# Kernel optimization log

Hardware: AMD Instinct MI355X
Metric: run time of the kernel (lower is better)

The kernel has to match this reference:

```python
import jax, jax.numpy as jnp
import numpy as np

B, L, CIN, COUT, TEMB, N_MODES = 32, 8192, 64, 64, 256, 64
M = N_MODES // 2 + 1  # retained rfft modes = 33
EPS = 1e-5


def setup_inputs() -> dict:
    key = jax.random.key(0)
    ks = jax.random.split(key, 12)
    std_w = float(np.sqrt(1.0 / (2.0 * CIN)))
    # flax Dense default kernel init = lecun_normal ~ normal(std=1/sqrt(fan_in)); plain normal is fine for a reference
    return {
        "x": jax.random.normal(ks[0], (B, L, CIN), jnp.float32),
        "t_emb": jax.random.normal(ks[1], (B, TEMB), jnp.float32),
        # SpectralFreqTimeConv1D params
        "spec_w_real": jax.random.normal(ks[2], (M, CIN, COUT), jnp.float32) * std_w,
        "spec_w_imag": jax.random.normal(ks[3], (M, CIN, COUT), jnp.float32) * std_w,
        "dense_re": jax.random.normal(ks[4], (TEMB, M), jnp.float32) / np.sqrt(TEMB),
        "dense_im": jax.random.normal(ks[5], (TEMB, M), jnp.float32) / np.sqrt(TEMB),
        # TimeConv1D params
        "conv_kernel": jax.random.normal(ks[6], (CIN, COUT), jnp.float32) / np.sqrt(CIN),
        "conv_bias": jnp.zeros((COUT,), jnp.float32),
        "tc_weights": jax.random.normal(ks[7], (COUT, COUT), jnp.float32) * 0.01,  # nn.initializers.normal() stddev=0.01
        "psi_kernel": jax.random.normal(ks[8], (TEMB, 2 * COUT), jnp.float32) / np.sqrt(TEMB),
        # BatchNorm params
        "bn_scale": jnp.ones((COUT,), jnp.float32),
        "bn_bias": jnp.zeros((COUT,), jnp.float32),
    }


def reference(x, t_emb, spec_w_real, spec_w_imag, dense_re, dense_im,
              conv_kernel, conv_bias, tc_weights, psi_kernel, bn_scale, bn_bias):
    b, L_in, _ = x.shape
    n_freq = L_in // 2 + 1

    # ---- SpectralFreqTimeConv1D ----
    x_ft = jnp.fft.rfft(x, axis=-2, norm="forward")            # (b, n_freq, CIN) complex
    t_c = (t_emb @ dense_re) + 1j * (t_emb @ dense_im)         # (b, M) complex
    W = spec_w_real + 1j * spec_w_imag                          # (M, CIN, COUT) complex
    # diagonal-in-mode modulation: equivalent to the eye-based einsum chain
    out_m = t_c[:, :, None] * jnp.einsum("bmi,mio->bmo", x_ft[:, :M, :], W)  # (b, M, COUT)
    out_ft = jnp.zeros((b, n_freq, COUT), jnp.complex64).at[:, :M, :].set(out_m)
    x_spec = jnp.fft.irfft(out_ft, axis=-2, n=L_in, norm="forward")  # (b, L, COUT)

    # ---- TimeConv1D (residual branch) ----
    h = x @ conv_kernel + conv_bias                             # 1x1 conv: (b, L, COUT)
    psi = t_emb @ psi_kernel                                    # (b, 2*COUT)
    w_t, b_t = jnp.split(psi, 2, axis=-1)
    # einsum('ij,bjk,blk->bli', W, diag(w_t), h) == (h * w_t) @ W^T
    x_res = jnp.einsum("blj,ij->bli", h * w_t[:, None, :], tc_weights) + b_t[:, None, :]

    # ---- combine, batchnorm (training: batch stats), activation ----
    out = x_spec + x_res
    mean = out.mean(axis=(0, 1))
    var = out.var(axis=(0, 1))
    out = (out - mean) * jax.lax.rsqrt(var + EPS) * bn_scale + bn_bias
    return jax.nn.relu(out)
```

## Files before the change

### kernel.cpp

```cpp
#include <hip/hip_runtime.h>
#include <hip/hip_fp16.h>

typedef short short8 __attribute__((ext_vector_type(8)));
typedef float f32x4 __attribute__((ext_vector_type(4)));
typedef unsigned int u32;
typedef u32 u32x4 __attribute__((ext_vector_type(4)));
typedef unsigned short u16;

#define BB 32
#define LL 8192
#define TE 256
#define MM 33
#define INVL (1.0f/8192.0f)

#define TBLM_OFF 0
#define TTD_OFF  262144
#define VTB_OFF  589824
#define DD_OFF   720896
#define DD2_OFF  722944
#define BNP_OFF  731200

#define SRED2_OFF 4227072
#define VF_OFF    4491264

static __device__ __forceinline__ u16 f2b(float f) {
  u32 u = __float_as_uint(f);
  return (u16)((u + 0x7FFFu + ((u >> 16) & 1u)) >> 16);
}
static __device__ __forceinline__ u32 pk2(float lo, float hi) {
  return __builtin_amdgcn_perm(__float_as_uint(hi) + 0x8000u,
                               __float_as_uint(lo) + 0x8000u,
                               0x07060302u);
}
static __device__ __forceinline__ float fsin(float rev) {
  float r; asm("v_sin_f32 %0, %1" : "=v"(r) : "v"(rev)); return r;
}
static __device__ __forceinline__ float fcos(float rev) {
  float r; asm("v_cos_f32 %0, %1" : "=v"(r) : "v"(rev)); return r;
}


__global__ __launch_bounds__(256) void k_tbl(float* __restrict__ ws) {
  u16* tt = (u16*)ws + TTD_OFF * 2;
  int t = blockIdx.x * 256 + threadIdx.x;
  int m = (t >> 13) + 1, l = t & (LL - 1);
  float rev = (float)((m * l) & (LL - 1)) * INVL;
  int js = (m == 32) ? 0 : 32 + m;
  tt[m * LL + l]  = f2b(fcos(rev));
  tt[js * LL + l] = f2b(fsin(rev));
}

__global__ __launch_bounds__(512) void k_dft(const float* __restrict__ x,
                                             const float* __restrict__ ws,
                                             float* __restrict__ scr) {
  __shared__ __align__(16) u16 sX[2][64 * 136];
  __shared__ float sOnes[8 * 64];
  int tid = threadIdx.x;
  int b = blockIdx.x >> 5, chunk = blockIdx.x & 31;
  int l0 = chunk * 256;
  int w = tid >> 6, lane = tid & 63;
  const u16* tt = (const u16*)ws + TTD_OFF * 2;

  f32x4 acc[4];
#pragma unroll
  for (int ct = 0; ct < 4; ++ct) acc[ct] = (f32x4){0.f, 0.f, 0.f, 0.f};

  int arow = lane & 15;
  int kb = (lane >> 4) * 8;
  bool isg = (w >= 4);
  int gi = w - 4;
  int sc = tid & 63, lg = tid >> 6;

  float vx[16];
  float psum = 0.f;
#pragma unroll
  for (int i = 0; i < 16; ++i)
    vx[i] = x[(b * LL + l0 + lg * 16 + i) * 64 + sc];
  {
    u32 wv[8];
#pragma unroll
    for (int j = 0; j < 8; ++j) {
      wv[j] = pk2(vx[2 * j], vx[2 * j + 1]);
      psum += vx[2 * j] + vx[2 * j + 1];
    }
    u32x4* dst = (u32x4*)&sX[0][sc * 136 + lg * 16];
    dst[0] = (u32x4){wv[0], wv[1], wv[2], wv[3]};
    dst[1] = (u32x4){wv[4], wv[5], wv[6], wv[7]};
  }
  __syncthreads();

#pragma unroll
  for (int i = 0; i < 16; ++i)
    vx[i] = x[(b * LL + l0 + 128 + lg * 16 + i) * 64 + sc];

#pragma unroll
  for (int kk = 0; kk < 4; ++kk) {
    short8 a = isg
      ? *reinterpret_cast<const short8*>(&sX[0][(gi * 16 + arow) * 136 + kk * 32 + kb])
      : *reinterpret_cast<const short8*>(tt + (w * 16 + arow) * LL + l0 + kk * 32 + kb);
#pragma unroll
    for (int ct = 0; ct < 4; ++ct) {
      short8 bf = *reinterpret_cast<const short8*>(&sX[0][(ct * 16 + arow) * 136 + kk * 32 + kb]);
      acc[ct] = __builtin_amdgcn_mfma_f32_16x16x32_bf16(a, bf, acc[ct], 0, 0, 0);
    }
  }

  {
    u32 wv[8];
#pragma unroll
    for (int j = 0; j < 8; ++j) {
      wv[j] = pk2(vx[2 * j], vx[2 * j + 1]);
      psum += vx[2 * j] + vx[2 * j + 1];
    }
    u32x4* dst = (u32x4*)&sX[1][sc * 136 + lg * 16];
    dst[0] = (u32x4){wv[0], wv[1], wv[2], wv[3]};
    dst[1] = (u32x4){wv[4], wv[5], wv[6], wv[7]};
  }
  sOnes[tid >> 6 == lg ? tid : tid] = psum;
  __syncthreads();

#pragma unroll
  for (int kk = 0; kk < 4; ++kk) {
    short8 a = isg
      ? *reinterpret_cast<const short8*>(&sX[1][(gi * 16 + arow) * 136 + kk * 32 + kb])
      : *reinterpret_cast<const short8*>(tt + (w * 16 + arow) * LL + l0 + 128 + kk * 32 + kb);
#pragma unroll
    for (int ct = 0; ct < 4; ++ct) {
      short8 bf = *reinterpret_cast<const short8*>(&sX[1][(ct * 16 + arow) * 136 + kk * 32 + kb]);
      acc[ct] = __builtin_amdgcn_mfma_f32_16x16x32_bf16(a, bf, acc[ct], 0, 0, 0);
    }
  }

  int rowbase = isg ? (65 + gi * 16) : (w * 16);
  int rowb = (lane >> 4) * 4;
  u16* pp = (u16*)scr + (size_t)(b * 32 + chunk) * 129 * 64;
#pragma unroll
  for (int ct = 0; ct < 4; ++ct) {
    int col = ct * 16 + (lane & 15);
#pragma unroll
    for (int r = 0; r < 4; ++r)
      pp[(rowbase + rowb + r) * 64 + col] = __half_as_ushort(__float2half(acc[ct][r]));
  }
  if (tid < 64) {
    float s = 0.f;
#pragma unroll
    for (int g = 0; g < 8; ++g) s += sOnes[g * 64 + tid];
    pp[64 * 64 + tid] = __half_as_ushort(__float2half(s));
  }
}

__global__ __launch_bounds__(256) void k_red1(float* __restrict__ scr,
                                              float* __restrict__ ws) {
  int bid = blockIdx.x, tid = threadIdx.x;
  if (bid < 544) {
    int b = bid / 17, rx = bid % 17;
    int p = rx * 256 + tid;
    if (p >= 4128) return;
    const u32* pb = (const u32*)scr + (size_t)b * 32 * 4128;
    float a0 = 0.f, a1 = 0.f;
#pragma unroll 8
    for (int ch = 0; ch < 32; ++ch) {
      u32 u = pb[ch * 4128 + p];
      __half2 h2 = *reinterpret_cast<const __half2*>(&u);
      float2 f = __half22float2(h2);
      a0 += f.x; a1 += f.y;
    }
    *reinterpret_cast<float2*>(scr + SRED2_OFF + b * 8256 + 2 * p) =
        make_float2(a0, a1);
  } else {
    u16* tb = (u16*)ws;
    int t = (bid - 544) * 256 + tid;
    int l = t >> 5, m = (t & 31) + 1;
    float rev = (float)((m * l) & (LL - 1)) * INVL;
    int js = (m == 32) ? 0 : 32 + m;
    tb[l * 64 + m]  = f2b(fcos(rev));
    tb[l * 64 + js] = f2b(fsin(rev));
  }
}

__global__ __launch_bounds__(256) void k_vb(
    const float* __restrict__ t_emb, const float* __restrict__ dre,
    const float* __restrict__ dim_, const float* __restrict__ pk,
    const float* __restrict__ swr, const float* __restrict__ swi,
    const float* __restrict__ ck, const float* __restrict__ cbias,
    const float* __restrict__ tw, float* __restrict__ scr,
    float* __restrict__ ws) {
  __shared__ float smem[12352];
  int tid = threadIdx.x;

  if (blockIdx.x < 33) {
    int m = blockIdx.x;
    float2* sW = (float2*)smem;
    float2* sX = (float2*)(smem + 8192);
    float* sTcb = smem + 8192 + 4096;

    for (int idx = tid; idx < 8192; idx += 256) smem[idx] = t_emb[idx];
    __syncthreads();
    if (tid < 64) {
      int b = tid & 31;
      const float* dd = (tid < 32) ? dre : dim_;
      float a = 0.f;
#pragma unroll 8
      for (int j = 0; j < TE; ++j) a = fmaf(smem[b * 256 + j], dd[j * MM + m], a);
      sTcb[tid] = a;
    }
    __syncthreads();

    for (int idx = tid; idx < 4096; idx += 256)
      sW[idx] = make_float2(swr[m * 4096 + idx], swi[m * 4096 + idx]);
    for (int idx = tid; idx < 2048; idx += 256) {
      int b = idx >> 6, i = idx & 63;
      const float* sr = scr + SRED2_OFF + b * 8256;
      float xr, xi;
      if (m == 0)      { xr = sr[64 * 64 + i] * INVL;  xi = 0.f; }
      else if (m < 32) { xr = sr[m * 64 + i] * INVL;   xi = -sr[(32 + m) * 64 + i] * INVL; }
      else             { xr = sr[32 * 64 + i] * INVL;  xi = -sr[0 * 64 + i] * INVL; }
      sX[idx] = make_float2(xr, xi);
    }
    __syncthreads();

    int w = tid >> 6, lane = tid & 63;
    for (int p = 0; p < 8; ++p) {
      int b = p * 4 + w;
      float a0 = 0.f, a1 = 0.f, a2 = 0.f, a3 = 0.f;
#pragma unroll 16
      for (int i = 0; i < 64; ++i) {
        float2 wv = sW[i * 64 + lane];
        float2 xv = sX[b * 64 + i];
        a0 = fmaf(xv.x, wv.x, a0);
        a1 = fmaf(xv.y, wv.y, a1);
        a2 = fmaf(xv.x, wv.y, a2);
        a3 = fmaf(xv.y, wv.x, a3);
      }
      float ar = a0 - a1, ai = a2 + a3;
      float tcr = sTcb[b], tci = sTcb[32 + b];
      float cr = tcr * ar - tci * ai;
      float ci = tcr * ai + tci * ar;
      if (m == 0) {
        ws[DD2_OFF + b * 64 + lane] = cr;
      } else {
        float crr = 2.f * cr, cii = -2.f * ci;
        int js = (m == 32) ? 0 : 32 + m;
        u16* vtb = (u16*)ws + VTB_OFF * 2 + (b * 64 + lane) * 128;
        vtb[64 + m] = f2b(crr);
        vtb[64 + js] = f2b(cii);
        float* vf = scr + VF_OFF + b * 8192;
        vf[(64 + m) * 64 + lane] = crr;
        vf[(64 + js) * 64 + lane] = cii;
      }
    }
  } else {
    int b = blockIdx.x - 33;
    float* sCkT = smem;
    float* sPtw = smem + 4096;
    float* sTe  = smem + 8192;
    float* sPsi = smem + 8448;

    sTe[tid] = t_emb[b * 256 + tid];
    __syncthreads();
    if (tid < 128) {
      float a = 0.f;
#pragma unroll 8
      for (int j = 0; j < TE; ++j) a = fmaf(sTe[j], pk[j * 128 + tid], a);
      sPsi[tid] = a;
    }
    __syncthreads();
    for (int idx = tid; idx < 4096; idx += 256) {
      int c = idx >> 6, j = idx & 63;
      sCkT[j * 64 + c] = ck[idx];
      sPtw[idx] = sPsi[j] * tw[idx];
    }
    __syncthreads();

    u16* vtb = (u16*)ws + VTB_OFF * 2 + b * 64 * 128;
    float* vf = scr + VF_OFF + b * 8192;
    int lane = tid & 63, w = tid >> 6;
#pragma unroll 4
    for (int it = 0; it < 16; ++it) {
      int o = it * 4 + w;
      float a = 0.f;
#pragma unroll 16
      for (int j = 0; j < 64; ++j)
        a = fmaf(sCkT[j * 64 + lane], sPtw[o * 64 + j], a);
      vtb[o * 128 + lane] = f2b(a);
      vf[lane * 64 + o] = a;
    }
    if (tid < 64) {
      float a = 0.f;
      for (int j = 0; j < 64; ++j) a = fmaf(cbias[j], sPtw[tid * 64 + j], a);
      ws[DD_OFF + b * 64 + tid] = a + sPsi[64 + tid];
    }
  }
}

__global__ __launch_bounds__(256) void k_bn(const float* __restrict__ scr,
                                            float* __restrict__ ws) {
  __shared__ float sVx[64 * 64];
  __shared__ float sGx[64 * 64];
  __shared__ float sS[64 * 64];
  __shared__ float sSum[64];
  __shared__ float sP[4][2][64];
  int tid = threadIdx.x, b = blockIdx.x;
  const float* sr = scr + SRED2_OFF + b * 8256;
  const float* vf = scr + VF_OFF + b * 8192;

  for (int p = tid; p < 4096; p += 256) {
    sVx[p] = vf[p];
    sGx[p] = sr[65 * 64 + p];
    sS[p]  = sr[p];
  }
  if (tid < 64) sSum[tid] = sr[64 * 64 + tid];
  __syncthreads();

  int o = tid & 63, part = tid >> 6;
  float m1 = 0.f, q1 = 0.f, cross = 0.f, vt2 = 0.f;
  for (int ii = 0; ii < 16; ++ii) {
    int i = part * 16 + ii;
    float vx = sVx[i * 64 + o];
    m1 = fmaf(sSum[i], vx, m1);
    float w0 = 0.f, w1 = 0.f, c0 = 0.f, c1 = 0.f;
#pragma unroll
    for (int j = 0; j < 64; j += 2) {
      float va = sVx[j * 64 + o], vb = sVx[(j + 1) * 64 + o];
      w0 = fmaf(sGx[i * 64 + j], va, w0);
      w1 = fmaf(sGx[i * 64 + j + 1], vb, w1);
      c0 = fmaf(sS[i * 64 + j], va, c0);
      c1 = fmaf(sS[i * 64 + j + 1], vb, c1);
    }
    q1 = fmaf(vx, w0 + w1, q1);
    float vt = vf[(64 + i) * 64 + o];
    vt2 = fmaf(vt, vt, vt2);
    cross = fmaf(vt, c0 + c1, cross);
  }
  sP[part][0][o] = m1;
  sP[part][1][o] = q1 + 2.f * cross + 4096.f * vt2;
  __syncthreads();
  if (tid < 64) {
    float m = sP[0][0][tid] + sP[1][0][tid] + sP[2][0][tid] + sP[3][0][tid];
    float q = sP[0][1][tid] + sP[1][1][tid] + sP[2][1][tid] + sP[3][1][tid];
    float D = ws[DD_OFF + b * 64 + tid] + ws[DD2_OFF + b * 64 + tid];
    ws[BNP_OFF + b * 128 + tid]      = m + 8192.f * D;
    ws[BNP_OFF + b * 128 + 64 + tid] = q + 2.f * D * m + 8192.f * D * D;
  }
}

__global__ __launch_bounds__(256) void k_main(const float* __restrict__ x,
                                              const float* __restrict__ ws,
                                              const float* __restrict__ bns,
                                              const float* __restrict__ bnb,
                                              float* __restrict__ out) {
  __shared__ float sD[64];
  __shared__ float sA[64];
  __shared__ float sB[64];
  __shared__ float sPp[4][64];
  __shared__ float sPq[4][64];
  int tid = threadIdx.x, w = tid >> 6, lane = tid & 63;
  int b = blockIdx.x >> 6, rg = blockIdx.x & 63;
  const u16* wsu = (const u16*)ws;

  int kb = (lane >> 4) * 8;
  const u16* vtb = wsu + VTB_OFF * 2 + b * 64 * 128;
  short8 bf[4][4];
#pragma unroll
  for (int kk = 0; kk < 4; ++kk)
#pragma unroll
    for (int ct = 0; ct < 4; ++ct)
      bf[kk][ct] = *reinterpret_cast<const short8*>(
          vtb + (ct * 16 + (lane & 15)) * 128 + kk * 32 + kb);

  {
    int o = tid & 63, g = tid >> 6;
    float pm = 0.f, pq = 0.f;
#pragma unroll
    for (int r = 0; r < 8; ++r) {
      int bb = g * 8 + r;
      pm += ws[BNP_OFF + bb * 128 + o];
      pq += ws[BNP_OFF + bb * 128 + 64 + o];
    }
    sPp[g][o] = pm;
    sPq[g][o] = pq;
  }
  if (tid < 64) sD[tid] = ws[DD_OFF + b * 64 + tid] + ws[DD2_OFF + b * 64 + tid];
  __syncthreads();
  if (tid < 64) {
    const float inv_n = 1.f / (32.f * 8192.f);
    float mean = (sPp[0][tid] + sPp[1][tid] + sPp[2][tid] + sPp[3][tid]) * inv_n;
    float ex2  = (sPq[0][tid] + sPq[1][tid] + sPq[2][tid] + sPq[3][tid]) * inv_n;
    float var = ex2 - mean * mean;
    float istd = rsqrtf(var + 1e-5f);
    float al = istd * bns[tid];
    sA[tid] = al;
    sB[tid] = bnb[tid] - mean * al;
  }
  __syncthreads();

  const u16* tb = wsu;
  int rowb = (lane >> 4) * 4;
  int lbase = rg * 128 + w * 32;

#pragma unroll
  for (int rt = 0; rt < 2; ++rt) {
    int l = lbase + rt * 16 + (lane & 15);
    const float* xq = x + (b * LL + l) * 64;
    float4 u0 = *reinterpret_cast<const float4*>(xq + kb);
    float4 u1 = *reinterpret_cast<const float4*>(xq + kb + 4);
    float4 u2 = *reinterpret_cast<const float4*>(xq + 32 + kb);
    float4 u3 = *reinterpret_cast<const float4*>(xq + 32 + kb + 4);
    union { short8 s; u32 wv[4]; } A0, A1;
    A0.wv[0] = pk2(u0.x, u0.y); A0.wv[1] = pk2(u0.z, u0.w);
    A0.wv[2] = pk2(u1.x, u1.y); A0.wv[3] = pk2(u1.z, u1.w);
    A1.wv[0] = pk2(u2.x, u2.y); A1.wv[1] = pk2(u2.z, u2.w);
    A1.wv[2] = pk2(u3.x, u3.y); A1.wv[3] = pk2(u3.z, u3.w);
    short8 a2 = *reinterpret_cast<const short8*>(tb + l * 64 + kb);
    short8 a3 = *reinterpret_cast<const short8*>(tb + l * 64 + 32 + kb);

    f32x4 acc[4];
#pragma unroll
    for (int ct = 0; ct < 4; ++ct) acc[ct] = (f32x4){0.f, 0.f, 0.f, 0.f};
#pragma unroll
    for (int ct = 0; ct < 4; ++ct) {
      acc[ct] = __builtin_amdgcn_mfma_f32_16x16x32_bf16(A0.s, bf[0][ct], acc[ct], 0, 0, 0);
      acc[ct] = __builtin_amdgcn_mfma_f32_16x16x32_bf16(A1.s, bf[1][ct], acc[ct], 0, 0, 0);
      acc[ct] = __builtin_amdgcn_mfma_f32_16x16x32_bf16(a2, bf[2][ct], acc[ct], 0, 0, 0);
      acc[ct] = __builtin_amdgcn_mfma_f32_16x16x32_bf16(a3, bf[3][ct], acc[ct], 0, 0, 0);
    }
#pragma unroll
    for (int ct = 0; ct < 4; ++ct) {
      int o = ct * 16 + (lane & 15);
      float dd = sD[o], al = sA[o], be = sB[o];
#pragma unroll
      for (int r = 0; r < 4; ++r) {
        float v = acc[ct][r] + dd;
        out[(b * LL + lbase + rt * 16 + rowb + r) * 64 + o] =
            fmaxf(fmaf(v, al, be), 0.f);
      }
    }
  }
}

extern "C" void kernel_launch(void* const* d_in, const int* in_sizes, int n_in,
                              void* d_out, int out_size, void* d_ws, size_t ws_size,
                              hipStream_t stream) {
  const float* x     = (const float*)d_in[0];
  const float* t_emb = (const float*)d_in[1];
  const float* swr   = (const float*)d_in[2];
  const float* swi   = (const float*)d_in[3];
  const float* dre   = (const float*)d_in[4];
  const float* dim_  = (const float*)d_in[5];
  const float* ck    = (const float*)d_in[6];
  const float* cbias = (const float*)d_in[7];
  const float* tw    = (const float*)d_in[8];
  const float* pk    = (const float*)d_in[9];
  const float* bns   = (const float*)d_in[10];
  const float* bnb   = (const float*)d_in[11];
  float* ws  = (float*)d_ws;
  float* out = (float*)d_out;

  k_tbl<<<1024, 256, 0, stream>>>(ws);
  k_dft<<<1024, 512, 0, stream>>>(x, ws, out);
  k_red1<<<1568, 256, 0, stream>>>(out, ws);
  k_vb<<<65, 256, 0, stream>>>(t_emb, dre, dim_, pk, swr, swi,
                               ck, cbias, tw, out, ws);
  k_bn<<<32, 256, 0, stream>>>(out, ws);
  k_main<<<2048, 256, 0, stream>>>(x, ws, bns, bnb, out);
}
```

Baseline: 99.78 us.

## Replace partial-sum scratch and reduction kernel with float atomics into zeroed buffer

The DFT kernel now accumulates its per-chunk spectral partials straight into the fp32 reduction buffer with atomicAdd, instead of writing fp16 partials that a separate reduction kernel summed. That reduction kernel is removed. Its table-generation work and the zeroing of the accumulation buffer move into the existing table kernel, which gets a larger grid. This saves one kernel launch and the scratch write/read traffic, and keeps partials in fp32, but adds atomic contention (32 chunks per address) and makes the summation order nondeterministic.

Result: slower. 119.6 us (+19.8%).

```diff
diff --git a/kernel.cpp b/kernel.cpp
--- a/kernel.cpp
+++ b/kernel.cpp
@@ -1,5 +1,4 @@
 #include <hip/hip_runtime.h>
-#include <hip/hip_fp16.h>
 
 typedef short short8 __attribute__((ext_vector_type(8)));
 typedef float f32x4 __attribute__((ext_vector_type(4)));
@@ -40,14 +39,30 @@
 }
 
 
-__global__ __launch_bounds__(256) void k_tbl(float* __restrict__ ws) {
-  u16* tt = (u16*)ws + TTD_OFF * 2;
-  int t = blockIdx.x * 256 + threadIdx.x;
-  int m = (t >> 13) + 1, l = t & (LL - 1);
-  float rev = (float)((m * l) & (LL - 1)) * INVL;
-  int js = (m == 32) ? 0 : 32 + m;
-  tt[m * LL + l]  = f2b(fcos(rev));
-  tt[js * LL + l] = f2b(fsin(rev));
+__global__ __launch_bounds__(256) void k_tbl(float* __restrict__ ws,
+                                             float* __restrict__ scr) {
+  int bid = blockIdx.x, tid = threadIdx.x;
+  if (bid < 1024) {
+    u16* tt = (u16*)ws + TTD_OFF * 2;
+    int t = bid * 256 + tid;
+    int m = (t >> 13) + 1, l = t & (LL - 1);
+    float rev = (float)((m * l) & (LL - 1)) * INVL;
+    int js = (m == 32) ? 0 : 32 + m;
+    tt[m * LL + l]  = f2b(fcos(rev));
+    tt[js * LL + l] = f2b(fsin(rev));
+  } else if (bid < 2048) {
+    u16* tb = (u16*)ws;
+    int t = (bid - 1024) * 256 + tid;
+    int l = t >> 5, m = (t & 31) + 1;
+    float rev = (float)((m * l) & (LL - 1)) * INVL;
+    int js = (m == 32) ? 0 : 32 + m;
+    tb[l * 64 + m]  = f2b(fcos(rev));
+    tb[l * 64 + js] = f2b(fsin(rev));
+  } else {
+    int t = (bid - 2048) * 256 + tid;
+    float4* z = (float4*)(scr + SRED2_OFF);
+    z[t] = make_float4(0.f, 0.f, 0.f, 0.f);
+  }
 }
 
 __global__ __launch_bounds__(512) void k_dft(const float* __restrict__ x,
@@ -116,7 +131,7 @@
     dst[0] = (u32x4){wv[0], wv[1], wv[2], wv[3]};
     dst[1] = (u32x4){wv[4], wv[5], wv[6], wv[7]};
   }
-  sOnes[tid >> 6 == lg ? tid : tid] = psum;
+  sOnes[tid] = psum;
   __syncthreads();
 
 #pragma unroll
@@ -133,48 +148,19 @@
 
   int rowbase = isg ? (65 + gi * 16) : (w * 16);
   int rowb = (lane >> 4) * 4;
-  u16* pp = (u16*)scr + (size_t)(b * 32 + chunk) * 129 * 64;
+  float* sr2 = scr + SRED2_OFF + b * 8256;
 #pragma unroll
   for (int ct = 0; ct < 4; ++ct) {
     int col = ct * 16 + (lane & 15);
 #pragma unroll
     for (int r = 0; r < 4; ++r)
-      pp[(rowbase + rowb + r) * 64 + col] = __half_as_ushort(__float2half(acc[ct][r]));
+      atomicAdd(&sr2[(rowbase + rowb + r) * 64 + col], acc[ct][r]);
   }
   if (tid < 64) {
     float s = 0.f;
 #pragma unroll
     for (int g = 0; g < 8; ++g) s += sOnes[g * 64 + tid];
-    pp[64 * 64 + tid] = __half_as_ushort(__float2half(s));
-  }
-}
-
-__global__ __launch_bounds__(256) void k_red1(float* __restrict__ scr,
-                                              float* __restrict__ ws) {
-  int bid = blockIdx.x, tid = threadIdx.x;
-  if (bid < 544) {
-    int b = bid / 17, rx = bid % 17;
-    int p = rx * 256 + tid;
-    if (p >= 4128) return;
-    const u32* pb = (const u32*)scr + (size_t)b * 32 * 4128;
-    float a0 = 0.f, a1 = 0.f;
-#pragma unroll 8
-    for (int ch = 0; ch < 32; ++ch) {
-      u32 u = pb[ch * 4128 + p];
-      __half2 h2 = *reinterpret_cast<const __half2*>(&u);
-      float2 f = __half22float2(h2);
-      a0 += f.x; a1 += f.y;
-    }
-    *reinterpret_cast<float2*>(scr + SRED2_OFF + b * 8256 + 2 * p) =
-        make_float2(a0, a1);
-  } else {
-    u16* tb = (u16*)ws;
-    int t = (bid - 544) * 256 + tid;
-    int l = t >> 5, m = (t & 31) + 1;
-    float rev = (float)((m * l) & (LL - 1)) * INVL;
-    int js = (m == 32) ? 0 : 32 + m;
-    tb[l * 64 + m]  = f2b(fcos(rev));
-    tb[l * 64 + js] = f2b(fsin(rev));
+    atomicAdd(&sr2[64 * 64 + tid], s);
   }
 }
 
@@ -456,9 +442,8 @@
   float* ws  = (float*)d_ws;
   float* out = (float*)d_out;
 
-  k_tbl<<<1024, 256, 0, stream>>>(ws);
+  k_tbl<<<2306, 256, 0, stream>>>(ws, out);
   k_dft<<<1024, 512, 0, stream>>>(x, ws, out);
-  k_red1<<<1568, 256, 0, stream>>>(out, ws);
   k_vb<<<65, 256, 0, stream>>>(t_emb, dre, dim_, pk, swr, swi,
                                ck, cbias, tw, out, ws);
   k_bn<<<32, 256, 0, stream>>>(out, ws);
```
